# Kernel tuning notes

Hardware: AMD Instinct MI355X
Metric: run time of the kernel (lower is better)

Reference implementation:

```python
import jax, jax.numpy as jnp
import numpy as np


def conv2d(x, w, b, stride, pad):
    out = jax.lax.conv_general_dilated(
        x, w, (stride, stride), [(pad, pad), (pad, pad)],
        dimension_numbers=("NCHW", "OIHW", "NCHW"))
    return out + b[None, :, None, None]


def setup_inputs() -> dict:
    key = jax.random.key(0)
    ks = jax.random.split(key, 7)
    B, Cin, Cout = 4, 32, 64
    x = jax.random.normal(ks[0], (B, Cin, 256, 256), jnp.float32)
    prev_h = jax.random.normal(ks[1], (B, Cout, 320, 320), jnp.float32)
    prev_c = jax.random.normal(ks[2], (B, Cout, 320, 320), jnp.float32)
    Wc = jax.random.normal(ks[3], (Cout, Cin, 5, 5), jnp.float32) * 0.05
    bc = jax.random.normal(ks[4], (Cout,), jnp.float32) * 0.05
    Wg = jax.random.normal(ks[5], (4 * Cout, 2 * Cout, 3, 3), jnp.float32) * 0.05
    bg = jax.random.normal(ks[6], (4 * Cout,), jnp.float32) * 0.05
    return {"x": x, "prev_h": prev_h, "prev_c": prev_c,
            "Wc": Wc, "bc": bc, "Wg": Wg, "bg": bg,
            "ey": 64, "ex": 64, "eh": 256, "ew": 256}


def reference(x, prev_h, prev_c, Wc, bc, Wg, bg, ey, ex, eh, ew):
    # axis_scale = 1; state indices are event coords // 2
    ey2, ex2, eh2, ew2 = ey // 2, ex // 2, eh // 2, ew // 2
    pad = 1  # ConvLSTM kernel_size // 2 (external padding)

    # ConvLayer: stride-2 conv + ReLU
    x_conv = jax.nn.relu(conv2d(x, Wc, bc, stride=2, pad=2))  # [B,Cout,eh2,ew2]

    def crop_with_padding(arr):
        H, W = arr.shape[-2], arr.shape[-1]
        y0, y1 = max(0, ey2 - pad), min(H, ey2 + eh2 + pad)
        x0, x1 = max(0, ex2 - pad), min(W, ex2 + ew2 + pad)
        c = arr[..., y0:y1, x0:x1]
        pt, pl = max(0, pad - ey2), max(0, pad - ex2)
        pb, pr = max(0, ey2 + eh2 + pad - H), max(0, ex2 + ew2 + pad - W)
        if pt or pl or pb or pr:
            c = jnp.pad(c, ((0, 0), (0, 0), (pt, pb), (pl, pr)))
        return c

    h_crop = crop_with_padding(prev_h)  # [B,Cout,eh2+2,ew2+2]
    c_crop = crop_with_padding(prev_c)

    x_pad = jnp.pad(x_conv, ((0, 0), (0, 0), (pad, pad), (pad, pad)))
    stacked = jnp.concatenate([x_pad, h_crop], axis=1)  # [B,2*Cout,eh2+2,ew2+2]
    gates = conv2d(stacked, Wg, bg, stride=1, pad=0)    # [B,4*Cout,eh2,ew2]
    i_g, r_g, o_g, c_g = jnp.split(gates, 4, axis=1)

    prev_cell = c_crop[..., pad:-pad, pad:-pad]
    cell = jax.nn.sigmoid(r_g) * prev_cell + jax.nn.sigmoid(i_g) * jnp.tanh(c_g)
    hidden = jax.nn.sigmoid(o_g) * jnp.tanh(cell)

    new_h = prev_h.at[..., ey2:ey2 + eh2, ex2:ex2 + ew2].set(hidden)
    new_c = prev_c.at[..., ey2:ey2 + eh2, ex2:ex2 + ew2].set(cell)
    return (hidden, new_h, new_c)
```

## Files before the change

kernel.cpp:

```cpp
#include <hip/hip_runtime.h>
#include <math.h>


#define OFF_NEWH 4194304
#define OFF_NEWC 30408704

typedef __attribute__((ext_vector_type(8))) short bf16x8;
typedef __attribute__((ext_vector_type(4))) float f32x4;

__device__ __forceinline__ float sigm(float v) { return 1.0f / (1.0f + expf(-v)); }

__device__ __forceinline__ unsigned short f2bf(float f) {
    unsigned u = __builtin_bit_cast(unsigned, f);
    u = (u + 0x7FFFu + ((u >> 16) & 1u)) >> 16;
    return (unsigned short)u;
}

__global__ __launch_bounds__(256) void pack_wc(
    const float* __restrict__ Wc, unsigned short* __restrict__ Wp1)
{
    int i = blockIdx.x * 256 + threadIdx.x;
    if (i < 51200) {
        int tap = i >> 11;
        int rem = i & 2047;
        int co  = rem >> 5;
        int ci  = rem & 31;
        Wp1[i] = f2bf(Wc[(co * 32 + ci) * 25 + tap]);
    }
}

__global__ __launch_bounds__(256) void pack_wg(
    const float* __restrict__ Wg, unsigned short* __restrict__ Wp)
{
    int i = blockIdx.x * 256 + threadIdx.x;
    if (i < 294912) {
        int tap = i >> 15;
        int rem = i & 32767;
        int co  = rem >> 7;
        int ci  = rem & 127;
        Wp[i] = f2bf(Wg[(co * 128 + ci) * 9 + tap]);
    }
}

__global__ __launch_bounds__(256) void conv1_mfma(
    const float* __restrict__ x,
    const unsigned short* __restrict__ Wp1,
    const float* __restrict__ bc,
    unsigned short* __restrict__ xconv)
{
    __shared__ __align__(16) unsigned short patch[361 * 40];

    const int tid  = threadIdx.x;
    const int lane = tid & 63;
    const int wv   = tid >> 6;
    const int l15  = lane & 15;
    const int g    = lane >> 4;

    const int tile = blockIdx.x;
    const int ty0  = (tile >> 4) << 3;
    const int tx0  = (tile & 15) << 3;
    const int n    = blockIdx.y;

    const int iyBase = 2 * ty0 - 2;
    const int ixBase = 2 * tx0 - 2;

    for (int r = tid; r < 608; r += 256) {
        int ci  = r / 19;
        int iyl = r - ci * 19;
        int iy  = iyBase + iyl;
        unsigned short* dst = patch + iyl * (19 * 40) + ci;
        if (iy >= 0 && iy < 256) {
            const float* src = x + ((n * 32 + ci) * 256 + iy) * 256;
#pragma unroll
            for (int ixl = 0; ixl < 19; ++ixl) {
                int ix = ixBase + ixl;
                unsigned short v = 0;
                if (ix >= 0 && ix < 256) v = f2bf(src[ix]);
                dst[ixl * 40] = v;
            }
        } else {
#pragma unroll
            for (int ixl = 0; ixl < 19; ++ixl) dst[ixl * 40] = 0;
        }
    }
    __syncthreads();

    f32x4 acc[4];
#pragma unroll
    for (int cf = 0; cf < 4; ++cf)
#pragma unroll
        for (int e = 0; e < 4; ++e) acc[cf][e] = 0.f;

    const unsigned short* Abase = Wp1 + (wv * 16 + l15) * 32 + g * 8;
    const int posBase = (2 * (l15 >> 3)) * 19 + 2 * (l15 & 7);
    const unsigned short* Bbase = patch + posBase * 40 + g * 8;

#pragma unroll
    for (int tap = 0; tap < 25; ++tap) {
        const int ky = tap / 5, kx = tap % 5;
        bf16x8 a = *(const bf16x8*)(Abase + tap * 2048);
        const unsigned short* Bt = Bbase + (ky * 19 + kx) * 40;
#pragma unroll
        for (int cf = 0; cf < 4; ++cf) {
            bf16x8 b = *(const bf16x8*)(Bt + cf * (76 * 40));
            acc[cf] = __builtin_amdgcn_mfma_f32_16x16x32_bf16(a, b, acc[cf], 0, 0, 0);
        }
    }

#pragma unroll
    for (int cf = 0; cf < 4; ++cf) {
        int p  = cf * 16 + l15;
        int oh = ty0 + (p >> 3);
        int ow = tx0 + (p & 7);
#pragma unroll
        for (int r = 0; r < 4; ++r) {
            int co = wv * 16 + g * 4 + r;
            float v = acc[cf][r] + bc[co];
            v = fmaxf(v, 0.f);
            xconv[((n * 64 + co) * 128 + oh) * 128 + ow] = f2bf(v);
        }
    }
}

__global__ __launch_bounds__(256) void gates_mfma(
    const unsigned short* __restrict__ xconv,
    const float* __restrict__ prev_h,
    const float* __restrict__ prev_c,
    const unsigned short* __restrict__ Wp,
    const float* __restrict__ bg,
    float* __restrict__ out)
{
    __shared__ __align__(16) unsigned short patch[100 * 136];

    const int tid  = threadIdx.x;
    const int lane = tid & 63;
    const int wv   = tid >> 6;
    const int l15  = lane & 15;
    const int g    = lane >> 4;

    const int tile = blockIdx.x;
    const int ty0  = (tile >> 4) << 3;
    const int tx0  = (tile & 15) << 3;
    const int n    = blockIdx.y;

    for (int r = tid; r < 1280; r += 256) {
        int ci = r / 10;
        int y  = r - ci * 10;
        int sy = ty0 + y;
        if (ci < 64) {
            int yy = sy - 1;
            const unsigned short* src = xconv + (((n * 64 + ci) * 128 + yy) * 128);
            bool yok = (yy >= 0 && yy < 128);
#pragma unroll
            for (int xx = 0; xx < 10; ++xx) {
                int sx = tx0 + xx - 1;
                unsigned short v = 0;
                if (yok && sx >= 0 && sx < 128) v = src[sx];
                patch[(y * 10 + xx) * 136 + ci] = v;
            }
        } else {
            const float* src = prev_h + ((n * 64 + (ci - 64)) * 320 + (31 + sy)) * 320 + 31 + tx0;
#pragma unroll
            for (int xx = 0; xx < 10; ++xx)
                patch[(y * 10 + xx) * 136 + ci] = f2bf(src[xx]);
        }
    }
    __syncthreads();

    f32x4 acc[4][4];
#pragma unroll
    for (int i = 0; i < 4; ++i)
#pragma unroll
        for (int j = 0; j < 4; ++j)
#pragma unroll
            for (int e = 0; e < 4; ++e) acc[i][j][e] = 0.f;

    const int arow = wv * 16 + l15;
    const unsigned short* Abase = Wp + arow * 128 + g * 8;
    const int bb = (l15 >> 3) * 10 + (l15 & 7);

    for (int tap = 0; tap < 9; ++tap) {
        const int ky = tap / 3;
        const int kx = tap - ky * 3;
        const int koff = ky * 10 + kx;
        const unsigned short* At = Abase + tap * 32768;
        const unsigned short* Bt = patch + (bb + koff) * 136 + g * 8;
#pragma unroll
        for (int chunk = 0; chunk < 4; ++chunk) {
            bf16x8 a0 = *(const bf16x8*)(At + 0 * 8192 + chunk * 32);
            bf16x8 a1 = *(const bf16x8*)(At + 1 * 8192 + chunk * 32);
            bf16x8 a2 = *(const bf16x8*)(At + 2 * 8192 + chunk * 32);
            bf16x8 a3 = *(const bf16x8*)(At + 3 * 8192 + chunk * 32);
            const unsigned short* pb = Bt + chunk * 32;
            bf16x8 b0 = *(const bf16x8*)(pb + 0 * 2720);
            bf16x8 b1 = *(const bf16x8*)(pb + 1 * 2720);
            bf16x8 b2 = *(const bf16x8*)(pb + 2 * 2720);
            bf16x8 b3 = *(const bf16x8*)(pb + 3 * 2720);
            acc[0][0] = __builtin_amdgcn_mfma_f32_16x16x32_bf16(a0, b0, acc[0][0], 0, 0, 0);
            acc[0][1] = __builtin_amdgcn_mfma_f32_16x16x32_bf16(a0, b1, acc[0][1], 0, 0, 0);
            acc[0][2] = __builtin_amdgcn_mfma_f32_16x16x32_bf16(a0, b2, acc[0][2], 0, 0, 0);
            acc[0][3] = __builtin_amdgcn_mfma_f32_16x16x32_bf16(a0, b3, acc[0][3], 0, 0, 0);
            acc[1][0] = __builtin_amdgcn_mfma_f32_16x16x32_bf16(a1, b0, acc[1][0], 0, 0, 0);
            acc[1][1] = __builtin_amdgcn_mfma_f32_16x16x32_bf16(a1, b1, acc[1][1], 0, 0, 0);
            acc[1][2] = __builtin_amdgcn_mfma_f32_16x16x32_bf16(a1, b2, acc[1][2], 0, 0, 0);
            acc[1][3] = __builtin_amdgcn_mfma_f32_16x16x32_bf16(a1, b3, acc[1][3], 0, 0, 0);
            acc[2][0] = __builtin_amdgcn_mfma_f32_16x16x32_bf16(a2, b0, acc[2][0], 0, 0, 0);
            acc[2][1] = __builtin_amdgcn_mfma_f32_16x16x32_bf16(a2, b1, acc[2][1], 0, 0, 0);
            acc[2][2] = __builtin_amdgcn_mfma_f32_16x16x32_bf16(a2, b2, acc[2][2], 0, 0, 0);
            acc[2][3] = __builtin_amdgcn_mfma_f32_16x16x32_bf16(a2, b3, acc[2][3], 0, 0, 0);
            acc[3][0] = __builtin_amdgcn_mfma_f32_16x16x32_bf16(a3, b0, acc[3][0], 0, 0, 0);
            acc[3][1] = __builtin_amdgcn_mfma_f32_16x16x32_bf16(a3, b1, acc[3][1], 0, 0, 0);
            acc[3][2] = __builtin_amdgcn_mfma_f32_16x16x32_bf16(a3, b2, acc[3][2], 0, 0, 0);
            acc[3][3] = __builtin_amdgcn_mfma_f32_16x16x32_bf16(a3, b3, acc[3][3], 0, 0, 0);
        }
    }

#pragma unroll
    for (int cf = 0; cf < 4; ++cf) {
        int p  = cf * 16 + l15;
        int oh = ty0 + (p >> 3);
        int ow = tx0 + (p & 7);
#pragma unroll
        for (int r = 0; r < 4; ++r) {
            int c = wv * 16 + g * 4 + r;
            float ig = acc[0][cf][r] + bg[c];
            float rg = acc[1][cf][r] + bg[64 + c];
            float og = acc[2][cf][r] + bg[128 + c];
            float gg = acc[3][cf][r] + bg[192 + c];
            float pc = prev_c[((n * 64 + c) * 320 + (32 + oh)) * 320 + (32 + ow)];
            float cell = sigm(rg) * pc + sigm(ig) * tanhf(gg);
            float hid  = sigm(og) * tanhf(cell);
            out[((n * 64 + c) * 128 + oh) * 128 + ow] = hid;
            out[OFF_NEWH + ((n * 64 + c) * 320 + (32 + oh)) * 320 + (32 + ow)] = hid;
            out[OFF_NEWC + ((n * 64 + c) * 320 + (32 + oh)) * 320 + (32 + ow)] = cell;
        }
    }
}

__global__ __launch_bounds__(256) void copy_f4(
    const float4* __restrict__ src, float4* __restrict__ dst, int n4)
{
    int i = blockIdx.x * blockDim.x + threadIdx.x;
    int stride = gridDim.x * blockDim.x;
    for (; i < n4; i += stride) dst[i] = src[i];
}

extern "C" void kernel_launch(void* const* d_in, const int* in_sizes, int n_in,
                              void* d_out, int out_size, void* d_ws, size_t ws_size,
                              hipStream_t stream)
{
    const float* x      = (const float*)d_in[0];
    const float* prev_h = (const float*)d_in[1];
    const float* prev_c = (const float*)d_in[2];
    const float* Wc     = (const float*)d_in[3];
    const float* bc     = (const float*)d_in[4];
    const float* Wg     = (const float*)d_in[5];
    const float* bg     = (const float*)d_in[6];

    float* out = (float*)d_out;
    unsigned short* xconv_bf = (unsigned short*)d_ws;
    unsigned short* Wp       = xconv_bf + 4194304;
    unsigned short* Wp1      = Wp + 294912;

    const int n4 = 26214400 / 4;
    copy_f4<<<2048, 256, 0, stream>>>((const float4*)prev_h, (float4*)(out + OFF_NEWH), n4);
    copy_f4<<<2048, 256, 0, stream>>>((const float4*)prev_c, (float4*)(out + OFF_NEWC), n4);

    pack_wg<<<1152, 256, 0, stream>>>(Wg, Wp);
    pack_wc<<<200, 256, 0, stream>>>(Wc, Wp1);
    conv1_mfma<<<dim3(256, 4), 256, 0, stream>>>(x, Wp1, bc, xconv_bf);
    gates_mfma<<<dim3(256, 4), 256, 0, stream>>>(xconv_bf, prev_h, prev_c, Wp, bg, out);
}
```

Measured before the change: 622.8 us.

## Stage conv inputs in padded channel-last bf16 buffers for vectorized patch loads

Adds pre-pass kernels that transpose x into a zero-padded NHWC bf16 buffer and write the cropped prev_h into the upper channels of a padded NHWC buffer. conv1 then writes its ReLU output into the lower channels of that same buffer. Both MFMA kernels can now fill their LDS patches with 16-byte vector loads and no bounds checks, replacing the previous scalar strided gathers with per-element conversion. The cost is two extra kernels, two memsets of roughly 17 MB each, and more workspace traffic.

```diff
diff --git a/kernel.cpp b/kernel.cpp
--- a/kernel.cpp
+++ b/kernel.cpp
@@ -4,6 +4,10 @@
 
 #define OFF_NEWH 4194304
 #define OFF_NEWC 30408704
+#define S_ELEMS  8652800
+#define XP_OFF   8652800
+#define WP_OFF   17305600
+#define WP1_OFF  17600512
 
 typedef __attribute__((ext_vector_type(8))) short bf16x8;
 typedef __attribute__((ext_vector_type(4))) float f32x4;
@@ -14,6 +18,9 @@
     unsigned u = __builtin_bit_cast(unsigned, f);
     u = (u + 0x7FFFu + ((u >> 16) & 1u)) >> 16;
     return (unsigned short)u;
+}
+__device__ __forceinline__ unsigned pack2(float lo, float hi) {
+    return (unsigned)f2bf(lo) | ((unsigned)f2bf(hi) << 16);
 }
 
 __global__ __launch_bounds__(256) void pack_wc(
@@ -42,11 +49,53 @@
     }
 }
 
+__global__ __launch_bounds__(256) void xpose_x(
+    const float* __restrict__ x, unsigned short* __restrict__ Xp)
+{
+    __shared__ __align__(16) float lds[32 * 260];
+    const int y = blockIdx.x, n = blockIdx.y, tid = threadIdx.x;
+
+    for (int u = tid; u < 2048; u += 256) {
+        int c = u >> 6, x4 = (u & 63) << 2;
+        float4 v = *(const float4*)(x + (((n * 32 + c) * 256 + y) << 8) + x4);
+        *(float4*)(&lds[c * 260 + x4]) = v;
+    }
+    __syncthreads();
+
+    const int px = tid;
+    unsigned short* dst = Xp + (((n * 260) + (y + 2)) * 260 + (px + 2)) * 32;
+#pragma unroll
+    for (int q = 0; q < 4; ++q) {
+        uint4 w;
+        w.x = pack2(lds[(q * 8 + 0) * 260 + px], lds[(q * 8 + 1) * 260 + px]);
+        w.y = pack2(lds[(q * 8 + 2) * 260 + px], lds[(q * 8 + 3) * 260 + px]);
+        w.z = pack2(lds[(q * 8 + 4) * 260 + px], lds[(q * 8 + 5) * 260 + px]);
+        w.w = pack2(lds[(q * 8 + 6) * 260 + px], lds[(q * 8 + 7) * 260 + px]);
+        *(uint4*)(dst + q * 8) = w;
+    }
+}
+
+__global__ __launch_bounds__(256) void hconv(
+    const float* __restrict__ prev_h, unsigned short* __restrict__ S)
+{
+    const int sy = blockIdx.x, n = blockIdx.y, tid = threadIdx.x;
+    for (int u = tid; u < 1040; u += 256) {
+        int px = u >> 3, ch = u & 7;
+        const float* src = prev_h + (((n * 64 + ch * 8) * 320 + (31 + sy)) * 320) + 31 + px;
+        uint4 w;
+        w.x = pack2(src[0 * 102400], src[1 * 102400]);
+        w.y = pack2(src[2 * 102400], src[3 * 102400]);
+        w.z = pack2(src[4 * 102400], src[5 * 102400]);
+        w.w = pack2(src[6 * 102400], src[7 * 102400]);
+        *(uint4*)(S + (((n * 130 + sy) * 130 + px) << 7) + 64 + ch * 8) = w;
+    }
+}
+
 __global__ __launch_bounds__(256) void conv1_mfma(
-    const float* __restrict__ x,
+    const unsigned short* __restrict__ Xp,
     const unsigned short* __restrict__ Wp1,
     const float* __restrict__ bc,
-    unsigned short* __restrict__ xconv)
+    unsigned short* __restrict__ S)
 {
     __shared__ __align__(16) unsigned short patch[361 * 40];
 
@@ -61,27 +110,12 @@
     const int tx0  = (tile & 15) << 3;
     const int n    = blockIdx.y;
 
-    const int iyBase = 2 * ty0 - 2;
-    const int ixBase = 2 * tx0 - 2;
-
-    for (int r = tid; r < 608; r += 256) {
-        int ci  = r / 19;
-        int iyl = r - ci * 19;
-        int iy  = iyBase + iyl;
-        unsigned short* dst = patch + iyl * (19 * 40) + ci;
-        if (iy >= 0 && iy < 256) {
-            const float* src = x + ((n * 32 + ci) * 256 + iy) * 256;
-#pragma unroll
-            for (int ixl = 0; ixl < 19; ++ixl) {
-                int ix = ixBase + ixl;
-                unsigned short v = 0;
-                if (ix >= 0 && ix < 256) v = f2bf(src[ix]);
-                dst[ixl * 40] = v;
-            }
-        } else {
-#pragma unroll
-            for (int ixl = 0; ixl < 19; ++ixl) dst[ixl * 40] = 0;
-        }
+    for (int u = tid; u < 1444; u += 256) {
+        int pos = u >> 2, ch = u & 3;
+        int iyl = pos / 19, ixl = pos - iyl * 19;
+        const unsigned short* src =
+            Xp + (((n * 260) + 2 * ty0 + iyl) * 260 + 2 * tx0 + ixl) * 32 + ch * 8;
+        *(bf16x8*)(&patch[pos * 40 + ch * 8]) = *(const bf16x8*)src;
     }
     __syncthreads();
 
@@ -112,19 +146,20 @@
         int p  = cf * 16 + l15;
         int oh = ty0 + (p >> 3);
         int ow = tx0 + (p & 7);
-#pragma unroll
-        for (int r = 0; r < 4; ++r) {
-            int co = wv * 16 + g * 4 + r;
-            float v = acc[cf][r] + bc[co];
-            v = fmaxf(v, 0.f);
-            xconv[((n * 64 + co) * 128 + oh) * 128 + ow] = f2bf(v);
-        }
+        int co = wv * 16 + g * 4;
+        float v0 = fmaxf(acc[cf][0] + bc[co + 0], 0.f);
+        float v1 = fmaxf(acc[cf][1] + bc[co + 1], 0.f);
+        float v2 = fmaxf(acc[cf][2] + bc[co + 2], 0.f);
+        float v3 = fmaxf(acc[cf][3] + bc[co + 3], 0.f);
+        uint2 w;
+        w.x = pack2(v0, v1);
+        w.y = pack2(v2, v3);
+        *(uint2*)(S + (((n * 130 + 1 + oh) * 130 + 1 + ow) << 7) + co) = w;
     }
 }
 
 __global__ __launch_bounds__(256) void gates_mfma(
-    const unsigned short* __restrict__ xconv,
-    const float* __restrict__ prev_h,
+    const unsigned short* __restrict__ S,
     const float* __restrict__ prev_c,
     const unsigned short* __restrict__ Wp,
     const float* __restrict__ bg,
@@ -143,27 +178,12 @@
     const int tx0  = (tile & 15) << 3;
     const int n    = blockIdx.y;
 
-    for (int r = tid; r < 1280; r += 256) {
-        int ci = r / 10;
-        int y  = r - ci * 10;
-        int sy = ty0 + y;
-        if (ci < 64) {
-            int yy = sy - 1;
-            const unsigned short* src = xconv + (((n * 64 + ci) * 128 + yy) * 128);
-            bool yok = (yy >= 0 && yy < 128);
-#pragma unroll
-            for (int xx = 0; xx < 10; ++xx) {
-                int sx = tx0 + xx - 1;
-                unsigned short v = 0;
-                if (yok && sx >= 0 && sx < 128) v = src[sx];
-                patch[(y * 10 + xx) * 136 + ci] = v;
-            }
-        } else {
-            const float* src = prev_h + ((n * 64 + (ci - 64)) * 320 + (31 + sy)) * 320 + 31 + tx0;
-#pragma unroll
-            for (int xx = 0; xx < 10; ++xx)
-                patch[(y * 10 + xx) * 136 + ci] = f2bf(src[xx]);
-        }
+    for (int u = tid; u < 1600; u += 256) {
+        int pos = u >> 4, ch = u & 15;
+        int y = pos / 10, xx = pos - y * 10;
+        const unsigned short* src =
+            S + (((n * 130 + ty0 + y) * 130 + tx0 + xx) << 7) + ch * 8;
+        *(bf16x8*)(&patch[pos * 136 + ch * 8]) = *(const bf16x8*)src;
     }
     __syncthreads();
 
@@ -175,8 +195,7 @@
 #pragma unroll
             for (int e = 0; e < 4; ++e) acc[i][j][e] = 0.f;
 
-    const int arow = wv * 16 + l15;
-    const unsigned short* Abase = Wp + arow * 128 + g * 8;
+    const unsigned short* Abase = Wp + (wv * 16 + l15) * 128 + g * 8;
     const int bb = (l15 >> 3) * 10 + (l15 & 7);
 
     for (int tap = 0; tap < 9; ++tap) {
@@ -258,9 +277,14 @@
     const float* bg     = (const float*)d_in[6];
 
     float* out = (float*)d_out;
-    unsigned short* xconv_bf = (unsigned short*)d_ws;
-    unsigned short* Wp       = xconv_bf + 4194304;
-    unsigned short* Wp1      = Wp + 294912;
+    unsigned short* S   = (unsigned short*)d_ws;
+    unsigned short* Xp  = S + XP_OFF - 0;
+    unsigned short* Wp  = S + WP_OFF;
+    unsigned short* Wp1 = S + WP1_OFF;
+    Xp = S + S_ELEMS;
+
+    hipMemsetAsync(S,  0, (size_t)S_ELEMS * 2, stream);
+    hipMemsetAsync(Xp, 0, (size_t)S_ELEMS * 2, stream);
 
     const int n4 = 26214400 / 4;
     copy_f4<<<2048, 256, 0, stream>>>((const float4*)prev_h, (float4*)(out + OFF_NEWH), n4);
@@ -268,6 +292,8 @@
 
     pack_wg<<<1152, 256, 0, stream>>>(Wg, Wp);
     pack_wc<<<200, 256, 0, stream>>>(Wc, Wp1);
-    conv1_mfma<<<dim3(256, 4), 256, 0, stream>>>(x, Wp1, bc, xconv_bf);
-    gates_mfma<<<dim3(256, 4), 256, 0, stream>>>(xconv_bf, prev_h, prev_c, Wp, bg, out);
-}
+    xpose_x<<<dim3(256, 4), 256, 0, stream>>>(x, Xp);
+    hconv<<<dim3(130, 4), 256, 0, stream>>>(prev_h, S);
+    conv1_mfma<<<dim3(256, 4), 256, 0, stream>>>(Xp, Wp1, bc, S);
+    gates_mfma<<<dim3(256, 4), 256, 0, stream>>>(S, prev_c, Wp, bg, out);
+}
```

New measurement: 621.3 us. Within noise of the previous version (-0.2%).
